# Kernel optimization log

Hardware: AMD Instinct MI355X
Metric: run time of the kernel (lower is better)

## Reference

```python
import jax, jax.numpy as jnp
import numpy as np

B, S, D, H, L, V = 2, 512, 1024, 16, 12, 50257
HD = D // H
DFF = 4 * D


def _ln(x, g, b, eps=1e-5):
    m = jnp.mean(x, axis=-1, keepdims=True)
    v = jnp.var(x, axis=-1, keepdims=True)
    return (x - m) * jax.lax.rsqrt(v + eps) * g + b


def setup_inputs() -> dict:
    key = jax.random.key(0)
    ks = jax.random.split(key, 32)
    sc = 0.02
    n = lambda k, shape: (jax.random.normal(k, shape, dtype=jnp.float32) * sc)
    inp = {
        "input_ids": jax.random.randint(ks[0], (B, S), 0, V, dtype=jnp.int64),
        "attention_mask": jnp.ones((B, S), dtype=jnp.float32),
        "image_hidden_states": jax.random.normal(ks[1], (B, D), dtype=jnp.float32),
        # token embedding table (also used for position embeds and tied lm_head, as in source)
        "wte": n(ks[2], (V, D)),
        # feature_space_transformation_nn: Linear(1024,1024) -> ReLU -> Linear(1024,1024)
        "ft_W1": n(ks[3], (D, D)), "ft_b1": jnp.zeros((D,), jnp.float32),
        "ft_W2": n(ks[4], (D, D)), "ft_b2": jnp.zeros((D,), jnp.float32),
        # per-layer params, stacked on leading L dim
        "ln1_g": jnp.ones((L, D), jnp.float32), "ln1_b": jnp.zeros((L, D), jnp.float32),
        "Wattn": n(ks[5], (L, D, 3 * D)), "battn": jnp.zeros((L, 3 * D), jnp.float32),
        "Wuk": n(ks[6], (L, D, D)), "buk": jnp.zeros((L, D), jnp.float32),
        "Wuv": n(ks[7], (L, D, D)), "buv": jnp.zeros((L, D), jnp.float32),
        "Wproj": n(ks[8], (L, D, D)), "bproj": jnp.zeros((L, D), jnp.float32),
        "ln2_g": jnp.ones((L, D), jnp.float32), "ln2_b": jnp.zeros((L, D), jnp.float32),
        "Wfc": n(ks[9], (L, D, DFF)), "bfc": jnp.zeros((L, DFF), jnp.float32),
        "Wfc2": n(ks[10], (L, DFF, D)), "bfc2": jnp.zeros((L, D), jnp.float32),
        "lnf_g": jnp.ones((D,), jnp.float32), "lnf_b": jnp.zeros((D,), jnp.float32),
    }
    return inp


def _forward(input_ids, attention_mask, image_hidden_states, wte,
             ft_W1, ft_b1, ft_W2, ft_b2,
             ln1_g, ln1_b, Wattn, battn, Wuk, buk, Wuv, buv, Wproj, bproj,
             ln2_g, ln2_b, Wfc, bfc, Wfc2, bfc2, lnf_g, lnf_b):
    # image feature transformation: Linear -> ReLU -> Linear
    img = jax.nn.relu(image_hidden_states @ ft_W1 + ft_b1) @ ft_W2 + ft_b2  # [B,D]

    # NOTE: source uses wte (not wpe) for position embeddings — faithful reproduction
    h = wte[input_ids] + wte[jnp.arange(S)][None]  # [B,S,D]

    # extended attention mask with a prepended zero column for the image token
    mask_ext = (1.0 - attention_mask)[:, None, None, :] * -10000.0  # [B,1,1,S]
    mask_ext = jnp.concatenate([jnp.zeros((B, 1, 1, 1), mask_ext.dtype), mask_ext], axis=-1)  # [B,1,1,S+1]

    # causal mask over kv_len=S+1: query i sees keys j <= i+1 (image token always visible)
    causal = jnp.arange(S + 1)[None, :] <= (jnp.arange(S)[:, None] + 1)  # [S,S+1]

    def block(h, p):
        (l1g, l1b, Wa, ba, Wk, bk, Wv, bv, Wp, bp, l2g, l2b, Wf, bf, Wf2, bf2) = p
        x = _ln(h, l1g, l1b)
        qkv = x @ Wa + ba
        q, k, v = jnp.split(qkv, 3, axis=-1)  # each [B,S,D]
        ki = (img @ Wk + bk)[:, None, :]  # [B,1,D]
        vi = (img @ Wv + bv)[:, None, :]
        k = jnp.concatenate([ki, k], axis=1)  # [B,S+1,D]
        v = jnp.concatenate([vi, v], axis=1)
        sh = lambda t, n: t.reshape(B, n, H, HD).transpose(0, 2, 1, 3)
        qh, kh, vh = sh(q, S), sh(k, S + 1), sh(v, S + 1)
        s = jnp.einsum('bhqd,bhkd->bhqk', qh, kh) / jnp.sqrt(jnp.float32(HD))
        s = jnp.where(causal[None, None], s, jnp.float32(-10000.0))
        s = s + mask_ext
        a = jax.nn.softmax(s, axis=-1)
        o = jnp.einsum('bhqk,bhkd->bhqd', a, vh).transpose(0, 2, 1, 3).reshape(B, S, D)
        h = h + (o @ Wp + bp)
        x = _ln(h, l2g, l2b)
        h = h + (jax.nn.gelu(x @ Wf + bf, approximate=True) @ Wf2 + bf2)
        return h, None

    params = (ln1_g, ln1_b, Wattn, battn, Wuk, buk, Wuv, buv, Wproj, bproj,
              ln2_g, ln2_b, Wfc, bfc, Wfc2, bfc2)
    h, _ = jax.lax.scan(block, h, params)
    h = _ln(h, lnf_g, lnf_b)
    return h @ wte.T  # tied lm head -> [B,S,V]


def reference(input_ids, attention_mask, image_hidden_states, wte,
              ft_W1, ft_b1, ft_W2, ft_b2,
              ln1_g, ln1_b, Wattn, battn, Wuk, buk, Wuv, buv, Wproj, bproj,
              ln2_g, ln2_b, Wfc, bfc, Wfc2, bfc2, lnf_g, lnf_b):
    return _forward(input_ids, attention_mask, image_hidden_states, wte,
                    ft_W1, ft_b1, ft_W2, ft_b2,
                    ln1_g, ln1_b, Wattn, battn, Wuk, buk, Wuv, buv, Wproj, bproj,
                    ln2_g, ln2_b, Wfc, bfc, Wfc2, bfc2, lnf_g, lnf_b)
```

## Files before the change

### kernel.cpp

```cpp
#include <hip/hip_runtime.h>
#include <cstdint>


typedef __bf16 bf16x8 __attribute__((ext_vector_type(8)));
typedef __bf16 bf16x4 __attribute__((ext_vector_type(4)));
typedef float  f32x4  __attribute__((ext_vector_type(4)));

#define GLDS16(g, l) __builtin_amdgcn_global_load_lds( \
    (const __attribute__((address_space(1))) unsigned int*)(g), \
    (__attribute__((address_space(3))) unsigned int*)(l), 16, 0, 0)

#define SCHED_FENCE() __builtin_amdgcn_sched_barrier(0)

__device__ __forceinline__ float gelu_f(float x) {
    float u = 1.5957691216057308f * (x + 0.044715f * x * x * x);
    float e = __expf(u);
    float t = 1.0f - 2.0f / (e + 1.0f);
    return 0.5f * x * (1.0f + t);
}

__device__ __forceinline__ int fragoff(int row, int kh, int hi) {
    return row * 64 + ((kh * 32 + hi * 8) ^ ((row & 7) << 3));
}

__global__ __launch_bounds__(256) void tcvt_layer(
    const float* __restrict__ Wa, const float* __restrict__ Wp,
    const float* __restrict__ Wf, const float* __restrict__ Wf2,
    __bf16* __restrict__ oa, __bf16* __restrict__ op,
    __bf16* __restrict__ of, __bf16* __restrict__ of2)
{
    int id = blockIdx.x;
    const float* src; __bf16* dst; int K, N, kb, nb;
    if (id < 3072)      { src = Wa;  dst = oa;  K = 1024; N = 3072; kb = id & 31;  nb = id >> 5; }
    else if (id < 4096) { id -= 3072; src = Wp;  dst = op;  K = 1024; N = 1024; kb = id & 31;  nb = id >> 5; }
    else if (id < 8192) { id -= 4096; src = Wf;  dst = of;  K = 1024; N = 4096; kb = id & 31;  nb = id >> 5; }
    else                { id -= 8192; src = Wf2; dst = of2; K = 4096; N = 1024; kb = id & 127; nb = id >> 7; }
    const int k0 = kb * 32, n0 = nb * 32;
    __shared__ float tile[32][33];
    const int t = threadIdx.x;
    const int r = t >> 3, c4 = (t & 7) * 4;
    float4 v = *reinterpret_cast<const float4*>(src + (long)(k0 + r) * N + n0 + c4);
    tile[r][c4] = v.x; tile[r][c4 + 1] = v.y; tile[r][c4 + 2] = v.z; tile[r][c4 + 3] = v.w;
    __syncthreads();
    bf16x4 o;
    o[0] = (__bf16)tile[c4][r];
    o[1] = (__bf16)tile[c4 + 1][r];
    o[2] = (__bf16)tile[c4 + 2][r];
    o[3] = (__bf16)tile[c4 + 3][r];
    *reinterpret_cast<bf16x4*>(dst + (long)(n0 + r) * K + k0 + c4) = o;
}

__global__ __launch_bounds__(256) void wcvt(
    const float* __restrict__ wte, __bf16* __restrict__ out, long nvalid)
{
    long e = ((long)blockIdx.x * 256 + threadIdx.x) * 8;
    bf16x8 o;
    if (e < nvalid) {
        float4 a = *reinterpret_cast<const float4*>(wte + e);
        float4 b = *reinterpret_cast<const float4*>(wte + e + 4);
        o[0] = (__bf16)a.x; o[1] = (__bf16)a.y; o[2] = (__bf16)a.z; o[3] = (__bf16)a.w;
        o[4] = (__bf16)b.x; o[5] = (__bf16)b.y; o[6] = (__bf16)b.z; o[7] = (__bf16)b.w;
    } else {
        #pragma unroll
        for (int i = 0; i < 8; i++) o[i] = (__bf16)0.f;
    }
    *reinterpret_cast<bf16x8*>(out + e) = o;
}

__global__ __launch_bounds__(256) void gemv_part(
    const float* __restrict__ x, int xld,
    const float* __restrict__ W, long wzs,
    float* __restrict__ part, int K, int N)
{
    int jb = blockIdx.x, kz = blockIdx.y, z = blockIdx.z;
    int t = threadIdx.x;
    int j = (jb << 6) + (t & 63);
    int g = t >> 6;
    int klen = K / (gridDim.y * 4);
    int kbase = (kz * 4 + g) * klen;
    const float* Wp = W + (long)z * wzs + (long)kbase * N + j;
    const float* x0 = x + kbase;
    const float* x1 = x + xld + kbase;
    float a0 = 0.f, a1 = 0.f;
    for (int k = 0; k < klen; k++) {
        float wv = Wp[(long)k * N];
        a0 += x0[k] * wv;
        a1 += x1[k] * wv;
    }
    __shared__ float r0[4][64], r1[4][64];
    r0[g][t & 63] = a0; r1[g][t & 63] = a1;
    __syncthreads();
    if (t < 64) {
        a0 = r0[0][t] + r0[1][t] + r0[2][t] + r0[3][t];
        a1 = r1[0][t] + r1[1][t] + r1[2][t] + r1[3][t];
        long base = (long)(z * gridDim.y + kz) * 2 * N + (jb << 6) + t;
        part[base]     = a0;
        part[base + N] = a1;
    }
}

__global__ __launch_bounds__(256) void gemv_reduce(
    const float* __restrict__ part, const float* __restrict__ bias, long bzs,
    float* __restrict__ out, int N, int nz, int act)
{
    int idx = blockIdx.x * 256 + threadIdx.x;
    if (idx >= nz * 2 * N) return;
    int j  = idx % N;
    int bz = idx / N;
    int z  = bz >> 1;
    float s = bias[(long)z * bzs + j];
    const float* p = part + ((long)z * 8 * 2 + (bz & 1)) * N + j;
    #pragma unroll
    for (int kz = 0; kz < 8; kz++) s += p[(long)kz * 2 * N];
    if (act) s = fmaxf(s, 0.f);
    out[idx] = s;
}

__global__ __launch_bounds__(256) void gemv_kv_part(
    const float* __restrict__ img,
    const float* __restrict__ Wuk, const float* __restrict__ Wuv,
    float* __restrict__ part)
{
    int jb = blockIdx.x, kz = blockIdx.y, z = blockIdx.z;
    int t = threadIdx.x;
    int j = (jb << 6) + (t & 63);
    int g = t >> 6;
    int kbase = (kz * 4 + g) * 64;
    const float* W = (z < 12) ? (Wuk + (long)z * 1048576) : (Wuv + (long)(z - 12) * 1048576);
    const float* Wp = W + (long)kbase * 1024 + j;
    const float* x0 = img + kbase;
    const float* x1 = img + 1024 + kbase;
    float a0 = 0.f, a1 = 0.f;
    for (int k = 0; k < 64; k++) {
        float wv = Wp[(long)k * 1024];
        a0 += x0[k] * wv;
        a1 += x1[k] * wv;
    }
    __shared__ float r0[4][64], r1[4][64];
    r0[g][t & 63] = a0; r1[g][t & 63] = a1;
    __syncthreads();
    if (t < 64) {
        a0 = r0[0][t] + r0[1][t] + r0[2][t] + r0[3][t];
        a1 = r1[0][t] + r1[1][t] + r1[2][t] + r1[3][t];
        long base = (long)(z * 4 + kz) * 2 * 1024 + (jb << 6) + t;
        part[base]        = a0;
        part[base + 1024] = a1;
    }
}

__global__ __launch_bounds__(256) void gemv_kv_reduce(
    const float* __restrict__ part,
    const float* __restrict__ buk, const float* __restrict__ buv,
    float* __restrict__ imgk, float* __restrict__ imgv)
{
    int idx = blockIdx.x * 256 + threadIdx.x;
    int z = idx >> 11;
    int bsel = (idx >> 10) & 1;
    int j = idx & 1023;
    float s = (z < 12) ? buk[z * 1024 + j] : buv[(z - 12) * 1024 + j];
    const float* p = part + ((long)z * 4 * 2 + bsel) * 1024 + j;
    #pragma unroll
    for (int kz = 0; kz < 4; kz++) s += p[(long)kz * 2 * 1024];
    if (z < 12) imgk[z * 2048 + bsel * 1024 + j] = s;
    else        imgv[(z - 12) * 2048 + bsel * 1024 + j] = s;
}

__global__ __launch_bounds__(256) void embed_ln(
    const int* __restrict__ ids, const float* __restrict__ wte,
    float* __restrict__ h, __bf16* __restrict__ xb,
    const float* __restrict__ g, const float* __restrict__ b)
{
    int row = blockIdx.x;
    int s = row & 511;
    int t = threadIdx.x;
    long id = ids[row];
    float4 v1 = reinterpret_cast<const float4*>(wte + id * 1024)[t];
    float4 v2 = reinterpret_cast<const float4*>(wte + (long)s * 1024)[t];
    float4 v; v.x = v1.x + v2.x; v.y = v1.y + v2.y; v.z = v1.z + v2.z; v.w = v1.w + v2.w;
    reinterpret_cast<float4*>(h + (long)row * 1024)[t] = v;

    float s1 = v.x + v.y + v.z + v.w;
    float s2 = v.x * v.x + v.y * v.y + v.z * v.z + v.w * v.w;
    #pragma unroll
    for (int o = 32; o >= 1; o >>= 1) { s1 += __shfl_xor(s1, o); s2 += __shfl_xor(s2, o); }
    __shared__ float r1[4], r2[4];
    int w = t >> 6;
    if ((t & 63) == 0) { r1[w] = s1; r2[w] = s2; }
    __syncthreads();
    s1 = r1[0] + r1[1] + r1[2] + r1[3];
    s2 = r2[0] + r2[1] + r2[2] + r2[3];
    float mean = s1 * (1.0f / 1024.0f);
    float var  = s2 * (1.0f / 1024.0f) - mean * mean;
    float rstd = rsqrtf(var + 1e-5f);
    float4 gg = reinterpret_cast<const float4*>(g)[t];
    float4 bb = reinterpret_cast<const float4*>(b)[t];
    bf16x4 o;
    o[0] = (__bf16)((v.x - mean) * rstd * gg.x + bb.x);
    o[1] = (__bf16)((v.y - mean) * rstd * gg.y + bb.y);
    o[2] = (__bf16)((v.z - mean) * rstd * gg.z + bb.z);
    o[3] = (__bf16)((v.w - mean) * rstd * gg.w + bb.w);
    *reinterpret_cast<bf16x4*>(xb + (long)row * 1024 + t * 4) = o;
}

__global__ __launch_bounds__(256) void ln_k(
    const float* __restrict__ in, __bf16* __restrict__ out,
    const float* __restrict__ g, const float* __restrict__ b)
{
    int row = blockIdx.x, t = threadIdx.x;
    float4 v = reinterpret_cast<const float4*>(in + (long)row * 1024)[t];
    float s1 = v.x + v.y + v.z + v.w;
    float s2 = v.x * v.x + v.y * v.y + v.z * v.z + v.w * v.w;
    #pragma unroll
    for (int o = 32; o >= 1; o >>= 1) { s1 += __shfl_xor(s1, o); s2 += __shfl_xor(s2, o); }
    __shared__ float r1[4], r2[4];
    int w = t >> 6;
    if ((t & 63) == 0) { r1[w] = s1; r2[w] = s2; }
    __syncthreads();
    s1 = r1[0] + r1[1] + r1[2] + r1[3];
    s2 = r2[0] + r2[1] + r2[2] + r2[3];
    float mean = s1 * (1.0f / 1024.0f);
    float var  = s2 * (1.0f / 1024.0f) - mean * mean;
    float rstd = rsqrtf(var + 1e-5f);
    float4 gg = reinterpret_cast<const float4*>(g)[t];
    float4 bb = reinterpret_cast<const float4*>(b)[t];
    bf16x4 o;
    o[0] = (__bf16)((v.x - mean) * rstd * gg.x + bb.x);
    o[1] = (__bf16)((v.y - mean) * rstd * gg.y + bb.y);
    o[2] = (__bf16)((v.z - mean) * rstd * gg.z + bb.z);
    o[3] = (__bf16)((v.w - mean) * rstd * gg.w + bb.w);
    *reinterpret_cast<bf16x4*>(out + (long)row * 1024 + t * 4) = o;
}

template<int NP>
__global__ __launch_bounds__(256) void lnadd_k(
    float* __restrict__ h, const float* __restrict__ part,
    const float* __restrict__ bias,
    const float* __restrict__ g, const float* __restrict__ b,
    __bf16* __restrict__ out)
{
    int row = blockIdx.x, t = threadIdx.x;
    long off = (long)row * 1024 + t * 4;
    float4 v = *reinterpret_cast<const float4*>(h + off);
    #pragma unroll
    for (int sp = 0; sp < NP; sp++) {
        float4 pv = *reinterpret_cast<const float4*>(part + sp * 1048576L + off);
        v.x += pv.x; v.y += pv.y; v.z += pv.z; v.w += pv.w;
    }
    float4 bi = reinterpret_cast<const float4*>(bias)[t];
    v.x += bi.x; v.y += bi.y; v.z += bi.z; v.w += bi.w;
    *reinterpret_cast<float4*>(h + off) = v;

    float s1 = v.x + v.y + v.z + v.w;
    float s2 = v.x * v.x + v.y * v.y + v.z * v.z + v.w * v.w;
    #pragma unroll
    for (int o = 32; o >= 1; o >>= 1) { s1 += __shfl_xor(s1, o); s2 += __shfl_xor(s2, o); }
    __shared__ float r1[4], r2[4];
    int w = t >> 6;
    if ((t & 63) == 0) { r1[w] = s1; r2[w] = s2; }
    __syncthreads();
    s1 = r1[0] + r1[1] + r1[2] + r1[3];
    s2 = r2[0] + r2[1] + r2[2] + r2[3];
    float mean = s1 * (1.0f / 1024.0f);
    float var  = s2 * (1.0f / 1024.0f) - mean * mean;
    float rstd = rsqrtf(var + 1e-5f);
    float4 gg = reinterpret_cast<const float4*>(g)[t];
    float4 bb = reinterpret_cast<const float4*>(b)[t];
    bf16x4 o;
    o[0] = (__bf16)((v.x - mean) * rstd * gg.x + bb.x);
    o[1] = (__bf16)((v.y - mean) * rstd * gg.y + bb.y);
    o[2] = (__bf16)((v.z - mean) * rstd * gg.z + bb.z);
    o[3] = (__bf16)((v.w - mean) * rstd * gg.w + bb.w);
    *reinterpret_cast<bf16x4*>(out + off) = o;
}

template<int OUTBF16, int ACT, int NBOUND, int PARTIAL>
__global__ __launch_bounds__(256) void gemm128(
    const __bf16* __restrict__ A, const __bf16* __restrict__ Bt,
    const float* __restrict__ bias, void* __restrict__ C,
    int N, int K, int GM, int GN, int NS)
{
    const int total = GM * GN * NS;
    const int q = total >> 3, r = total & 7;
    const int x = blockIdx.x & 7, jj = blockIdx.x >> 3;
    const int w0 = (x < r) ? x * (q + 1) + jj : r * (q + 1) + (x - r) * q + jj;
    const int sp = w0 / (GM * GN);
    const int rem = w0 - sp * (GM * GN);
    const int m0 = (rem % GM) * 128;
    const int n0 = (rem / GM) * 128;

    __shared__ __bf16 As[2][128 * 64];
    __shared__ __bf16 Bs[2][128 * 64];
    const int t = threadIdx.x;
    const int wv = t >> 6, lane = t & 63;
    const int lo = lane & 15, hi = lane >> 4;
    const int wr = wv >> 1, wc = wv & 1;

    f32x4 acc[4][4] = {};

    const int srow = t >> 3;
    const int skx  = (((t & 7) ^ (srow & 7)) << 3);
    const int sldst = t * 8;
    #define ST128(bf, kk) do { \
        _Pragma("unroll") \
        for (int i = 0; i < 4; i++) \
            GLDS16(A + (long)(m0 + i * 32 + srow) * K + (kk) + skx, &As[bf][i * 2048 + sldst]); \
        _Pragma("unroll") \
        for (int i = 0; i < 4; i++) \
            GLDS16(Bt + (long)(n0 + i * 32 + srow) * K + (kk) + skx, &Bs[bf][i * 2048 + sldst]); \
    } while (0)

    const int Ksp = K / NS;
    const int kbeg = sp * Ksp;
    const int T = Ksp >> 6;

    ST128(0, kbeg);
    int cur = 0;
    for (int it = 0; it < T; it++) {
        if (it + 1 < T) {
            ST128(cur ^ 1, kbeg + (it + 1) * 64);
            asm volatile("s_waitcnt vmcnt(8)" ::: "memory");
        } else {
            asm volatile("s_waitcnt vmcnt(0)" ::: "memory");
        }
        SCHED_FENCE();
        __builtin_amdgcn_s_barrier();
        SCHED_FENCE();

        #pragma unroll
        for (int kh = 0; kh < 2; kh++) {
            bf16x8 afr[4], bfr[4];
            #pragma unroll
            for (int mi = 0; mi < 4; mi++)
                afr[mi] = *reinterpret_cast<const bf16x8*>(&As[cur][fragoff(wr * 64 + mi * 16 + lo, kh, hi)]);
            #pragma unroll
            for (int ni = 0; ni < 4; ni++)
                bfr[ni] = *reinterpret_cast<const bf16x8*>(&Bs[cur][fragoff(wc * 64 + ni * 16 + lo, kh, hi)]);
            #pragma unroll
            for (int mi = 0; mi < 4; mi++)
                #pragma unroll
                for (int ni = 0; ni < 4; ni++)
                    acc[mi][ni] = __builtin_amdgcn_mfma_f32_16x16x32_bf16(afr[mi], bfr[ni], acc[mi][ni], 0, 0, 0);
        }

        SCHED_FENCE();
        __builtin_amdgcn_s_barrier();
        SCHED_FENCE();
        cur ^= 1;
    }
    #undef ST128

    const long coff = PARTIAL ? (long)sp * GM * 128 * N : 0;
    #pragma unroll
    for (int mi = 0; mi < 4; mi++)
        #pragma unroll
        for (int ni = 0; ni < 4; ni++) {
            int col = n0 + wc * 64 + ni * 16 + lo;
            if (NBOUND && col >= N) continue;
            float bv = (!PARTIAL && bias) ? bias[col] : 0.f;
            #pragma unroll
            for (int rr = 0; rr < 4; rr++) {
                int row = m0 + wr * 64 + mi * 16 + hi * 4 + rr;
                float v = acc[mi][ni][rr] + bv;
                if (ACT) v = gelu_f(v);
                if (OUTBF16) ((__bf16*)C)[(long)row * N + col] = (__bf16)v;
                else         ((float*)C)[coff + (long)row * N + col] = v;
            }
        }
}

template<int BN, int OUTBF16, int ACT, int PARTIAL>
__global__ __launch_bounds__(256) void gemm64(
    const __bf16* __restrict__ A, const __bf16* __restrict__ Bt,
    const float* __restrict__ bias, void* __restrict__ C,
    int N, int K, int GM, int GN, int NS)
{
    constexpr int NB = BN / 32;
    const int total = GM * GN * NS;
    const int q = total >> 3, r = total & 7;
    const int x = blockIdx.x & 7, jj = blockIdx.x >> 3;
    const int w0 = (x < r) ? x * (q + 1) + jj : r * (q + 1) + (x - r) * q + jj;
    const int sp = w0 / (GM * GN);
    const int rem = w0 - sp * (GM * GN);
    const int m0 = (rem % GM) * 64;
    const int n0 = (rem / GM) * BN;

    __shared__ __bf16 As[2][64 * 64];
    __shared__ __bf16 Bs[2][BN * 64];
    const int t = threadIdx.x;
    const int wv = t >> 6, lane = t & 63;
    const int lo = lane & 15, hi = lane >> 4;
    const int wr = wv >> 1, wc = wv & 1;

    f32x4 acc[2][NB] = {};

    const int srow = t >> 3;
    const int skx  = (((t & 7) ^ (srow & 7)) << 3);
    const int sldst = t * 8;
    #define ST64(bf, kk) do { \
        _Pragma("unroll") \
        for (int i = 0; i < 2; i++) \
            GLDS16(A + (long)(m0 + i * 32 + srow) * K + (kk) + skx, &As[bf][i * 2048 + sldst]); \
        _Pragma("unroll") \
        for (int i = 0; i < NB; i++) \
            GLDS16(Bt + (long)(n0 + i * 32 + srow) * K + (kk) + skx, &Bs[bf][i * 2048 + sldst]); \
    } while (0)

    const int Ksp = K / NS;
    const int kbeg = sp * Ksp;
    const int T = Ksp >> 6;

    ST64(0, kbeg);
    int cur = 0;
    for (int it = 0; it < T; it++) {
        if (it + 1 < T) {
            ST64(cur ^ 1, kbeg + (it + 1) * 64);
            if constexpr (NB == 4) asm volatile("s_waitcnt vmcnt(6)" ::: "memory");
            else                   asm volatile("s_waitcnt vmcnt(4)" ::: "memory");
        } else {
            asm volatile("s_waitcnt vmcnt(0)" ::: "memory");
        }
        SCHED_FENCE();
        __builtin_amdgcn_s_barrier();
        SCHED_FENCE();

        #pragma unroll
        for (int kh = 0; kh < 2; kh++) {
            bf16x8 afr[2], bfr[NB];
            #pragma unroll
            for (int mi = 0; mi < 2; mi++)
                afr[mi] = *reinterpret_cast<const bf16x8*>(&As[cur][fragoff(wr * 32 + mi * 16 + lo, kh, hi)]);
            #pragma unroll
            for (int ni = 0; ni < NB; ni++)
                bfr[ni] = *reinterpret_cast<const bf16x8*>(&Bs[cur][fragoff(wc * (BN / 2) + ni * 16 + lo, kh, hi)]);
            #pragma unroll
            for (int mi = 0; mi < 2; mi++)
                #pragma unroll
                for (int ni = 0; ni < NB; ni++)
                    acc[mi][ni] = __builtin_amdgcn_mfma_f32_16x16x32_bf16(afr[mi], bfr[ni], acc[mi][ni], 0, 0, 0);
        }

        SCHED_FENCE();
        __builtin_amdgcn_s_barrier();
        SCHED_FENCE();
        cur ^= 1;
    }
    #undef ST64

    const long coff = PARTIAL ? (long)sp * GM * 64 * N : 0;
    #pragma unroll
    for (int mi = 0; mi < 2; mi++)
        #pragma unroll
        for (int ni = 0; ni < NB; ni++) {
            int col = n0 + wc * (BN / 2) + ni * 16 + lo;
            float bv = (!PARTIAL && bias) ? bias[col] : 0.f;
            #pragma unroll
            for (int rr = 0; rr < 4; rr++) {
                int row = m0 + wr * 32 + mi * 16 + hi * 4 + rr;
                float v = acc[mi][ni][rr] + bv;
                if (ACT) v = gelu_f(v);
                if (OUTBF16) ((__bf16*)C)[(long)row * N + col] = (__bf16)v;
                else         ((float*)C)[coff + (long)row * N + col] = v;
            }
        }
}

template<int OUTBF16, int ACT, int RES>
__global__ __launch_bounds__(256) void gemm_bb(
    const __bf16* __restrict__ A, const __bf16* __restrict__ Bt,
    const float* __restrict__ bias, const float* __restrict__ res,
    void* __restrict__ C, int N, int K)
{
    __shared__ __bf16 As[64 * 32];
    __shared__ __bf16 Bs[64 * 32];
    const int t = threadIdx.x;
    const int m0 = blockIdx.x * 64;
    const int n0 = blockIdx.y * 64;
    const int w = t >> 6, lane = t & 63;
    const int lo = lane & 15, hi = lane >> 4;
    const int wr = w >> 1, wc = w & 1;

    f32x4 acc[2][2] = {};

    for (int k0 = 0; k0 < K; k0 += 32) {
        __syncthreads();
        GLDS16(A  + (long)(m0 + (t >> 2)) * K + k0 + ((t & 3) << 3), &As[t * 8]);
        GLDS16(Bt + (long)(n0 + (t >> 2)) * K + k0 + ((t & 3) << 3), &Bs[t * 8]);
        __syncthreads();
        bf16x8 afr[2], bfr[2];
        #pragma unroll
        for (int mi = 0; mi < 2; mi++)
            afr[mi] = *reinterpret_cast<const bf16x8*>(&As[(wr * 32 + mi * 16 + lo) * 32 + hi * 8]);
        #pragma unroll
        for (int ni = 0; ni < 2; ni++)
            bfr[ni] = *reinterpret_cast<const bf16x8*>(&Bs[(wc * 32 + ni * 16 + lo) * 32 + hi * 8]);
        #pragma unroll
        for (int mi = 0; mi < 2; mi++)
            #pragma unroll
            for (int ni = 0; ni < 2; ni++)
                acc[mi][ni] = __builtin_amdgcn_mfma_f32_16x16x32_bf16(afr[mi], bfr[ni], acc[mi][ni], 0, 0, 0);
    }

    #pragma unroll
    for (int mi = 0; mi < 2; mi++)
        #pragma unroll
        for (int ni = 0; ni < 2; ni++) {
            int col = n0 + wc * 32 + ni * 16 + lo;
            float bv = bias ? bias[col] : 0.f;
            #pragma unroll
            for (int rr = 0; rr < 4; rr++) {
                int row = m0 + wr * 32 + mi * 16 + hi * 4 + rr;
                float v = acc[mi][ni][rr] + bv;
                if (ACT) v = gelu_f(v);
                if (RES) v += res[(long)row * N + col];
                if (OUTBF16) ((__bf16*)C)[(long)row * N + col] = (__bf16)v;
                else         ((float*)C)[(long)row * N + col] = v;
            }
        }
}

__global__ __launch_bounds__(256) void gemm_lm(
    const __bf16* __restrict__ A, const float* __restrict__ Wt,
    float* __restrict__ C, int N, int K)
{
    __shared__ __bf16 As[128 * 32];
    __shared__ __bf16 Bs[128 * 32];
    const int t = threadIdx.x;
    const int m0 = blockIdx.x * 128;
    const int n0 = blockIdx.y * 128;
    const int w = t >> 6, lane = t & 63;
    const int lo = lane & 15, hi = lane >> 4;
    const int wr = w >> 1, wc = w & 1;

    f32x4 acc[4][4] = {};

    for (int k0 = 0; k0 < K; k0 += 32) {
        __syncthreads();
        #pragma unroll
        for (int i = 0; i < 2; i++) {
            int c = i * 256 + t;
            GLDS16(A + (long)(m0 + (c >> 2)) * K + k0 + ((c & 3) << 3), &As[c * 8]);
        }
        #pragma unroll
        for (int i = 0; i < 2; i++) {
            int c = i * 256 + t;
            int nr = n0 + (c >> 2);
            bf16x8 bv;
            if (nr < N) {
                const float* wp = Wt + (long)nr * K + k0 + ((c & 3) << 3);
                float4 b0 = *reinterpret_cast<const float4*>(wp);
                float4 b1 = *reinterpret_cast<const float4*>(wp + 4);
                bv[0] = (__bf16)b0.x; bv[1] = (__bf16)b0.y; bv[2] = (__bf16)b0.z; bv[3] = (__bf16)b0.w;
                bv[4] = (__bf16)b1.x; bv[5] = (__bf16)b1.y; bv[6] = (__bf16)b1.z; bv[7] = (__bf16)b1.w;
            } else {
                #pragma unroll
                for (int qq = 0; qq < 8; qq++) bv[qq] = (__bf16)0.f;
            }
            *reinterpret_cast<bf16x8*>(&Bs[c * 8]) = bv;
        }
        __syncthreads();
        bf16x8 afr[4], bfr[4];
        #pragma unroll
        for (int mi = 0; mi < 4; mi++)
            afr[mi] = *reinterpret_cast<const bf16x8*>(&As[(wr * 64 + mi * 16 + lo) * 32 + hi * 8]);
        #pragma unroll
        for (int ni = 0; ni < 4; ni++)
            bfr[ni] = *reinterpret_cast<const bf16x8*>(&Bs[(wc * 64 + ni * 16 + lo) * 32 + hi * 8]);
        #pragma unroll
        for (int mi = 0; mi < 4; mi++)
            #pragma unroll
            for (int ni = 0; ni < 4; ni++)
                acc[mi][ni] = __builtin_amdgcn_mfma_f32_16x16x32_bf16(afr[mi], bfr[ni], acc[mi][ni], 0, 0, 0);
    }

    #pragma unroll
    for (int mi = 0; mi < 4; mi++)
        #pragma unroll
        for (int ni = 0; ni < 4; ni++) {
            int col = n0 + wc * 64 + ni * 16 + lo;
            if (col < N) {
                #pragma unroll
                for (int rr = 0; rr < 4; rr++) {
                    int row = m0 + wr * 64 + mi * 16 + hi * 4 + rr;
                    C[(long)row * N + col] = acc[mi][ni][rr];
                }
            }
        }
}

__global__ __launch_bounds__(256) void attn_mfma(
    const __bf16* __restrict__ qkv,
    const float* __restrict__ imgk, const float* __restrict__ imgv,
    const float* __restrict__ amask, __bf16* __restrict__ out)
{
    const int qb = blockIdx.x;
    const int h  = blockIdx.y;
    const int b  = blockIdx.z;
    const int t = threadIdx.x, w = t >> 6, lane = t & 63;
    const int lo = lane & 15, hi = lane >> 4;

    __shared__ __bf16 Ks[64][72];
    __shared__ __bf16 Vt[64][72];
    __shared__ __bf16 Ps[4][16][72];
    __shared__ float kimg_s[64];
    __shared__ float amv_s[64];

    const int kr8 = t >> 2, kd8 = (t & 3) * 16;
    const int vr8 = t & 63, vd8 = (t >> 6) * 16;

    const __bf16* qrow = qkv + (long)(b * 512 + qb * 64 + w * 16 + lo) * 3072 + h * 64;
    bf16x8 qf0 = *reinterpret_cast<const bf16x8*>(qrow + hi * 8);
    bf16x8 qf1 = *reinterpret_cast<const bf16x8*>(qrow + 32 + hi * 8);

    if (t < 64) kimg_s[t] = imgk[b * 1024 + h * 64 + t];
    __syncthreads();

    float simg = 0.f;
    #pragma unroll
    for (int i = 0; i < 8; i++)
        simg += (float)qf0[i] * kimg_s[hi * 8 + i] + (float)qf1[i] * kimg_s[32 + hi * 8 + i];
    simg += __shfl_xor(simg, 16);
    simg += __shfl_xor(simg, 32);
    simg *= 0.125f;

    float pimg[4], l_part[4];
    f32x4 o_acc[4];
    #pragma unroll
    for (int rr = 0; rr < 4; rr++) {
        pimg[rr] = __expf(__shfl(simg, hi * 4 + rr));
        l_part[rr] = 0.f;
    }
    #pragma unroll
    for (int df = 0; df < 4; df++) {
        float vi = imgv[b * 1024 + h * 64 + df * 16 + lo];
        #pragma unroll
        for (int rr = 0; rr < 4; rr++) o_acc[df][rr] = pimg[rr] * vi;
    }

    bf16x8 ck0, ck1, cv0, cv1;
    {
        const __bf16* ks = qkv + (long)(b * 512 + kr8) * 3072 + 1024 + h * 64 + kd8;
        ck0 = *reinterpret_cast<const bf16x8*>(ks);
        ck1 = *reinterpret_cast<const bf16x8*>(ks + 8);
        const __bf16* vs = qkv + (long)(b * 512 + vr8) * 3072 + 2048 + h * 64 + vd8;
        cv0 = *reinterpret_cast<const bf16x8*>(vs);
        cv1 = *reinterpret_cast<const bf16x8*>(vs + 8);
    }

    for (int kb = 0; kb <= qb; kb++) {
        bf16x8 nk0, nk1, nv0, nv1;
        const bool more = (kb < qb);
        if (more) {
            const __bf16* ks = qkv + (long)(b * 512 + (kb + 1) * 64 + kr8) * 3072 + 1024 + h * 64 + kd8;
            nk0 = *reinterpret_cast<const bf16x8*>(ks);
            nk1 = *reinterpret_cast<const bf16x8*>(ks + 8);
            const __bf16* vs = qkv + (long)(b * 512 + (kb + 1) * 64 + vr8) * 3072 + 2048 + h * 64 + vd8;
            nv0 = *reinterpret_cast<const bf16x8*>(vs);
            nv1 = *reinterpret_cast<const bf16x8*>(vs + 8);
        }
        __syncthreads();
        *reinterpret_cast<bf16x8*>(&Ks[kr8][kd8])     = ck0;
        *reinterpret_cast<bf16x8*>(&Ks[kr8][kd8 + 8]) = ck1;
        #pragma unroll
        for (int i = 0; i < 8; i++) { Vt[vd8 + i][vr8] = cv0[i]; Vt[vd8 + 8 + i][vr8] = cv1[i]; }
        if (t < 64) amv_s[t] = (1.0f - amask[b * 512 + kb * 64 + t]) * -10000.0f;
        __syncthreads();

        f32x4 sf[4];
        #pragma unroll
        for (int js = 0; js < 4; js++) {
            bf16x8 kf0 = *reinterpret_cast<const bf16x8*>(&Ks[js * 16 + lo][hi * 8]);
            bf16x8 kf1 = *reinterpret_cast<const bf16x8*>(&Ks[js * 16 + lo][32 + hi * 8]);
            f32x4 a = {};
            a = __builtin_amdgcn_mfma_f32_16x16x32_bf16(qf0, kf0, a, 0, 0, 0);
            a = __builtin_amdgcn_mfma_f32_16x16x32_bf16(qf1, kf1, a, 0, 0, 0);
            sf[js] = a;
        }
        #pragma unroll
        for (int js = 0; js < 4; js++) {
            float amv = amv_s[js * 16 + lo];
            #pragma unroll
            for (int rr = 0; rr < 4; rr++) {
                float sv = sf[js][rr] * 0.125f + amv;
                if (kb == qb) {
                    int qrw = w * 16 + hi * 4 + rr;
                    if (js * 16 + lo > qrw) sv = -10000.0f + amv;
                }
                float p = __expf(sv);
                l_part[rr] += p;
                Ps[w][hi * 4 + rr][js * 16 + lo] = (__bf16)p;
            }
        }
        #pragma unroll
        for (int jb = 0; jb < 2; jb++) {
            bf16x8 pf = *reinterpret_cast<const bf16x8*>(&Ps[w][lo][jb * 32 + hi * 8]);
            #pragma unroll
            for (int df = 0; df < 4; df++) {
                bf16x8 vf = *reinterpret_cast<const bf16x8*>(&Vt[df * 16 + lo][jb * 32 + hi * 8]);
                o_acc[df] = __builtin_amdgcn_mfma_f32_16x16x32_bf16(pf, vf, o_acc[df], 0, 0, 0);
            }
        }
        if (more) { ck0 = nk0; ck1 = nk1; cv0 = nv0; cv1 = nv1; }
    }

    float linv[4];
    #pragma unroll
    for (int rr = 0; rr < 4; rr++) {
        float ls = l_part[rr];
        #pragma unroll
        for (int off = 1; off < 16; off <<= 1) ls += __shfl_xor(ls, off);
        linv[rr] = 1.0f / (pimg[rr] + ls);
    }
    #pragma unroll
    for (int df = 0; df < 4; df++)
        #pragma unroll
        for (int rr = 0; rr < 4; rr++) {
            long row = b * 512 + qb * 64 + w * 16 + hi * 4 + rr;
            out[row * 1024 + h * 64 + df * 16 + lo] = (__bf16)(o_acc[df][rr] * linv[rr]);
        }
}

extern "C" void kernel_launch(void* const* d_in, const int* in_sizes, int n_in,
                              void* d_out, int out_size, void* d_ws, size_t ws_size,
                              hipStream_t stream) {
    (void)in_sizes; (void)n_in; (void)out_size;
    const int*   ids   = (const int*)d_in[0];
    const float* amask = (const float*)d_in[1];
    const float* ihs   = (const float*)d_in[2];
    const float* wte   = (const float*)d_in[3];
    const float* ftW1  = (const float*)d_in[4];
    const float* ftb1  = (const float*)d_in[5];
    const float* ftW2  = (const float*)d_in[6];
    const float* ftb2  = (const float*)d_in[7];
    const float* ln1g  = (const float*)d_in[8];
    const float* ln1b  = (const float*)d_in[9];
    const float* Wattn = (const float*)d_in[10];
    const float* battn = (const float*)d_in[11];
    const float* Wuk   = (const float*)d_in[12];
    const float* buk   = (const float*)d_in[13];
    const float* Wuv   = (const float*)d_in[14];
    const float* buv   = (const float*)d_in[15];
    const float* Wproj = (const float*)d_in[16];
    const float* bproj = (const float*)d_in[17];
    const float* ln2g  = (const float*)d_in[18];
    const float* ln2b  = (const float*)d_in[19];
    const float* Wfc   = (const float*)d_in[20];
    const float* bfc   = (const float*)d_in[21];
    const float* Wfc2  = (const float*)d_in[22];
    const float* bfc2  = (const float*)d_in[23];
    const float* lnfg  = (const float*)d_in[24];
    const float* lnfb  = (const float*)d_in[25];
    float* out = (float*)d_out;

    const long VP = 50304;
    char* base = (char*)d_ws;
    float* ftmp  = (float*)(base);
    float* img   = (float*)(base + (1 << 13));
    float* imgk  = (float*)(base + (1 << 14));
    float* imgv  = (float*)(base + 114688);
    float* part  = (float*)(base + 212992);
    float* h     = (float*)(base + 1048576);
    char* p = base + 5 * 1048576;
    __bf16* xb    = (__bf16*)p; p += 2 * 1048576;
    __bf16* qkvb  = (__bf16*)p; p += 6 * 1048576;
    __bf16* attob = (__bf16*)p; p += 2 * 1048576;
    __bf16* ffb   = (__bf16*)p; p += 8 * 1048576;
    __bf16* wtA   = (__bf16*)p; p += 6 * 1048576;
    __bf16* wtP   = (__bf16*)p; p += 2 * 1048576;
    __bf16* wtF   = (__bf16*)p; p += 8 * 1048576;
    __bf16* wtF2  = (__bf16*)p; p += 8 * 1048576;
    __bf16* wteb  = (__bf16*)p;
    size_t need1 = (size_t)(p - base) + (size_t)VP * 1024 * 2;
    float* part_g = (float*)(base + need1);
    size_t need2 = need1 + 4 * 1048576 * sizeof(float);
    const bool big_ws  = (ws_size >= need1);
    const bool big_ws2 = (ws_size >= need2);

    dim3 b256(256);

    gemv_part<<<dim3(16, 8, 1), b256, 0, stream>>>(ihs, 1024, ftW1, 0, part, 1024, 1024);
    gemv_reduce<<<dim3(8), b256, 0, stream>>>(part, ftb1, 0, ftmp, 1024, 1, 1);
    gemv_part<<<dim3(16, 8, 1), b256, 0, stream>>>(ftmp, 1024, ftW2, 0, part, 1024, 1024);
    gemv_reduce<<<dim3(8), b256, 0, stream>>>(part, ftb2, 0, img, 1024, 1, 0);
    gemv_kv_part<<<dim3(16, 4, 24), b256, 0, stream>>>(img, Wuk, Wuv, part);
    gemv_kv_reduce<<<dim3(192), b256, 0, stream>>>(part, buk, buv, imgk, imgv);

    embed_ln<<<dim3(1024), b256, 0, stream>>>(ids, wte, h, xb, ln1g, ln1b);

    for (int l = 0; l < 12; l++) {
        tcvt_layer<<<dim3(12288), b256, 0, stream>>>(
            Wattn + (long)l * 1024 * 3072, Wproj + (long)l * 1024 * 1024,
            Wfc + (long)l * 1024 * 4096, Wfc2 + (long)l * 4096 * 1024,
            wtA, wtP, wtF, wtF2);

        gemm64<128, 1, 0, 0><<<dim3(384), b256, 0, stream>>>(
            xb, wtA, battn + l * 3072, qkvb, 3072, 1024, 16, 24, 1);
        attn_mfma<<<dim3(8, 16, 2), b256, 0, stream>>>(
            qkvb, imgk + l * 2048, imgv + l * 2048, amask, attob);

        const float* ng = (l < 11) ? (ln1g + (l + 1) * 1024) : lnfg;
        const float* nb = (l < 11) ? (ln1b + (l + 1) * 1024) : lnfb;
        if (big_ws2) {
            gemm64<64, 0, 0, 1><<<dim3(512), b256, 0, stream>>>(
                attob, wtP, nullptr, part_g, 1024, 1024, 16, 16, 2);
            lnadd_k<2><<<dim3(1024), b256, 0, stream>>>(
                h, part_g, bproj + l * 1024, ln2g + l * 1024, ln2b + l * 1024, xb);
            gemm64<128, 1, 1, 0><<<dim3(512), b256, 0, stream>>>(
                xb, wtF, bfc + l * 4096, ffb, 4096, 1024, 16, 32, 1);
            gemm64<128, 0, 0, 1><<<dim3(512), b256, 0, stream>>>(
                ffb, wtF2, nullptr, part_g, 1024, 4096, 16, 8, 4);
            lnadd_k<4><<<dim3(1024), b256, 0, stream>>>(
                h, part_g, bfc2 + l * 1024, ng, nb, xb);
        } else {
            gemm_bb<0, 0, 1><<<dim3(16, 16), b256, 0, stream>>>(
                attob, wtP, bproj + l * 1024, h, h, 1024, 1024);
            ln_k<<<dim3(1024), b256, 0, stream>>>(h, xb, ln2g + l * 1024, ln2b + l * 1024);
            gemm64<128, 1, 1, 0><<<dim3(512), b256, 0, stream>>>(
                xb, wtF, bfc + l * 4096, ffb, 4096, 1024, 16, 32, 1);
            gemm_bb<0, 0, 1><<<dim3(16, 16), b256, 0, stream>>>(
                ffb, wtF2, bfc2 + l * 1024, h, h, 1024, 4096);
            ln_k<<<dim3(1024), b256, 0, stream>>>(h, xb, ng, nb);
        }
    }

    if (big_ws) {
        wcvt<<<dim3((unsigned)(VP * 1024 / 2048)), b256, 0, stream>>>(wte, wteb, 50257L * 1024);
        gemm128<0, 0, 1, 0><<<dim3(3144), b256, 0, stream>>>(
            xb, wteb, nullptr, out, 50257, 1024, 8, 393, 1);
    } else {
        gemm_lm<<<dim3(8, 393), b256, 0, stream>>>(xb, wte, out, 50257, 1024);
    }
}
```

Before: 1.593 ms.

## Overlap weight conversion with attention and enlarge LM-head GEMM tiles

Next-layer weight transpose/convert (and the vocab embedding conversion on the final layer) are folded into the attention launch as extra blocks. This lets the conversion run alongside the small 256-block attention grid, using double-buffered converted-weight workspaces. The transpose kernel now works on 64x64 tiles, and the LM head uses a new 256x256-tile, 512-thread GEMM with padded vocab. The cost is more workspace, a larger shared-memory footprint for attention, and possible register pressure in the bigger GEMM.

```diff
diff --git a/kernel.cpp b/kernel.cpp
--- a/kernel.cpp
+++ b/kernel.cpp
@@ -23,48 +23,73 @@
     return row * 64 + ((kh * 32 + hi * 8) ^ ((row & 7) << 3));
 }
 
-__global__ __launch_bounds__(256) void tcvt_layer(
+__device__ __forceinline__ void tcvt_body(
+    int id, const float* __restrict__ Wa, const float* __restrict__ Wp,
+    const float* __restrict__ Wf, const float* __restrict__ Wf2,
+    __bf16* __restrict__ oa, __bf16* __restrict__ op,
+    __bf16* __restrict__ of, __bf16* __restrict__ of2, float* tile)
+{
+    const float* src; __bf16* dst; int K, N, kb, nb;
+    if (id < 768)       { src = Wa;  dst = oa;  K = 1024; N = 3072; kb = id & 15; nb = id >> 4; }
+    else if (id < 1024) { id -= 768;  src = Wp;  dst = op;  K = 1024; N = 1024; kb = id & 15; nb = id >> 4; }
+    else if (id < 2048) { id -= 1024; src = Wf;  dst = of;  K = 1024; N = 4096; kb = id & 15; nb = id >> 4; }
+    else                { id -= 2048; src = Wf2; dst = of2; K = 4096; N = 1024; kb = id & 63; nb = id >> 6; }
+    const int k0 = kb * 64, n0 = nb * 64;
+    const int t = threadIdx.x;
+    #pragma unroll
+    for (int i = 0; i < 4; i++) {
+        int r = i * 16 + (t >> 4), c = (t & 15) * 4;
+        float4 v = *reinterpret_cast<const float4*>(src + (long)(k0 + r) * N + n0 + c);
+        tile[r * 65 + c] = v.x; tile[r * 65 + c + 1] = v.y;
+        tile[r * 65 + c + 2] = v.z; tile[r * 65 + c + 3] = v.w;
+    }
+    __syncthreads();
+    const int nrow = t >> 2, kc = (t & 3) * 16;
+    bf16x8 o0, o1;
+    #pragma unroll
+    for (int i = 0; i < 8; i++) {
+        o0[i] = (__bf16)tile[(kc + i) * 65 + nrow];
+        o1[i] = (__bf16)tile[(kc + 8 + i) * 65 + nrow];
+    }
+    *reinterpret_cast<bf16x8*>(dst + (long)(n0 + nrow) * K + k0 + kc)     = o0;
+    *reinterpret_cast<bf16x8*>(dst + (long)(n0 + nrow) * K + k0 + kc + 8) = o1;
+}
+
+__device__ __forceinline__ void wcvt_body(
+    int id, const float* __restrict__ wte, __bf16* __restrict__ out, long nvalid)
+{
+    long base = (long)id * 8192 + threadIdx.x * 8;
+    #pragma unroll
+    for (int i = 0; i < 4; i++) {
+        long e = base + (long)i * 2048;
+        bf16x8 o;
+        if (e < nvalid) {
+            float4 a = *reinterpret_cast<const float4*>(wte + e);
+            float4 b = *reinterpret_cast<const float4*>(wte + e + 4);
+            o[0] = (__bf16)a.x; o[1] = (__bf16)a.y; o[2] = (__bf16)a.z; o[3] = (__bf16)a.w;
+            o[4] = (__bf16)b.x; o[5] = (__bf16)b.y; o[6] = (__bf16)b.z; o[7] = (__bf16)b.w;
+        } else {
+            #pragma unroll
+            for (int q = 0; q < 8; q++) o[q] = (__bf16)0.f;
+        }
+        *reinterpret_cast<bf16x8*>(out + e) = o;
+    }
+}
+
+__global__ __launch_bounds__(256) void tcvt_std(
     const float* __restrict__ Wa, const float* __restrict__ Wp,
     const float* __restrict__ Wf, const float* __restrict__ Wf2,
     __bf16* __restrict__ oa, __bf16* __restrict__ op,
     __bf16* __restrict__ of, __bf16* __restrict__ of2)
 {
-    int id = blockIdx.x;
-    const float* src; __bf16* dst; int K, N, kb, nb;
-    if (id < 3072)      { src = Wa;  dst = oa;  K = 1024; N = 3072; kb = id & 31;  nb = id >> 5; }
-    else if (id < 4096) { id -= 3072; src = Wp;  dst = op;  K = 1024; N = 1024; kb = id & 31;  nb = id >> 5; }
-    else if (id < 8192) { id -= 4096; src = Wf;  dst = of;  K = 1024; N = 4096; kb = id & 31;  nb = id >> 5; }
-    else                { id -= 8192; src = Wf2; dst = of2; K = 4096; N = 1024; kb = id & 127; nb = id >> 7; }
-    const int k0 = kb * 32, n0 = nb * 32;
-    __shared__ float tile[32][33];
-    const int t = threadIdx.x;
-    const int r = t >> 3, c4 = (t & 7) * 4;
-    float4 v = *reinterpret_cast<const float4*>(src + (long)(k0 + r) * N + n0 + c4);
-    tile[r][c4] = v.x; tile[r][c4 + 1] = v.y; tile[r][c4 + 2] = v.z; tile[r][c4 + 3] = v.w;
-    __syncthreads();
-    bf16x4 o;
-    o[0] = (__bf16)tile[c4][r];
-    o[1] = (__bf16)tile[c4 + 1][r];
-    o[2] = (__bf16)tile[c4 + 2][r];
-    o[3] = (__bf16)tile[c4 + 3][r];
-    *reinterpret_cast<bf16x4*>(dst + (long)(n0 + r) * K + k0 + c4) = o;
-}
-
-__global__ __launch_bounds__(256) void wcvt(
+    __shared__ float tile[64 * 65];
+    tcvt_body(blockIdx.x, Wa, Wp, Wf, Wf2, oa, op, of, of2, tile);
+}
+
+__global__ __launch_bounds__(256) void wcvt_std(
     const float* __restrict__ wte, __bf16* __restrict__ out, long nvalid)
 {
-    long e = ((long)blockIdx.x * 256 + threadIdx.x) * 8;
-    bf16x8 o;
-    if (e < nvalid) {
-        float4 a = *reinterpret_cast<const float4*>(wte + e);
-        float4 b = *reinterpret_cast<const float4*>(wte + e + 4);
-        o[0] = (__bf16)a.x; o[1] = (__bf16)a.y; o[2] = (__bf16)a.z; o[3] = (__bf16)a.w;
-        o[4] = (__bf16)b.x; o[5] = (__bf16)b.y; o[6] = (__bf16)b.z; o[7] = (__bf16)b.w;
-    } else {
-        #pragma unroll
-        for (int i = 0; i < 8; i++) o[i] = (__bf16)0.f;
-    }
-    *reinterpret_cast<bf16x8*>(out + e) = o;
+    wcvt_body(blockIdx.x, wte, out, nvalid);
 }
 
 __global__ __launch_bounds__(256) void gemv_part(
@@ -273,51 +298,44 @@
     *reinterpret_cast<bf16x4*>(out + off) = o;
 }
 
-template<int OUTBF16, int ACT, int NBOUND, int PARTIAL>
-__global__ __launch_bounds__(256) void gemm128(
+__global__ __launch_bounds__(512) void gemm256(
     const __bf16* __restrict__ A, const __bf16* __restrict__ Bt,
-    const float* __restrict__ bias, void* __restrict__ C,
-    int N, int K, int GM, int GN, int NS)
-{
-    const int total = GM * GN * NS;
+    float* __restrict__ C, int N, int K, int GM, int GN)
+{
+    const int total = GM * GN;
     const int q = total >> 3, r = total & 7;
     const int x = blockIdx.x & 7, jj = blockIdx.x >> 3;
     const int w0 = (x < r) ? x * (q + 1) + jj : r * (q + 1) + (x - r) * q + jj;
-    const int sp = w0 / (GM * GN);
-    const int rem = w0 - sp * (GM * GN);
-    const int m0 = (rem % GM) * 128;
-    const int n0 = (rem / GM) * 128;
-
-    __shared__ __bf16 As[2][128 * 64];
-    __shared__ __bf16 Bs[2][128 * 64];
+    const int m0 = (w0 % GM) * 256;
+    const int n0 = (w0 / GM) * 256;
+
+    __shared__ __bf16 As[2][256 * 64];
+    __shared__ __bf16 Bs[2][256 * 64];
     const int t = threadIdx.x;
-    const int wv = t >> 6, lane = t & 63;
+    const int wid = t >> 6, lane = t & 63;
     const int lo = lane & 15, hi = lane >> 4;
-    const int wr = wv >> 1, wc = wv & 1;
-
-    f32x4 acc[4][4] = {};
+    const int wr = wid >> 2, wc = wid & 3;
+
+    f32x4 acc[8][4] = {};
 
     const int srow = t >> 3;
     const int skx  = (((t & 7) ^ (srow & 7)) << 3);
     const int sldst = t * 8;
-    #define ST128(bf, kk) do { \
+    #define ST256(bf, kk) do { \
         _Pragma("unroll") \
         for (int i = 0; i < 4; i++) \
-            GLDS16(A + (long)(m0 + i * 32 + srow) * K + (kk) + skx, &As[bf][i * 2048 + sldst]); \
+            GLDS16(A + (long)(m0 + i * 64 + srow) * K + (kk) + skx, &As[bf][i * 4096 + sldst]); \
         _Pragma("unroll") \
         for (int i = 0; i < 4; i++) \
-            GLDS16(Bt + (long)(n0 + i * 32 + srow) * K + (kk) + skx, &Bs[bf][i * 2048 + sldst]); \
+            GLDS16(Bt + (long)(n0 + i * 64 + srow) * K + (kk) + skx, &Bs[bf][i * 4096 + sldst]); \
     } while (0)
 
-    const int Ksp = K / NS;
-    const int kbeg = sp * Ksp;
-    const int T = Ksp >> 6;
-
-    ST128(0, kbeg);
+    const int T = K >> 6;
+    ST256(0, 0);
     int cur = 0;
     for (int it = 0; it < T; it++) {
         if (it + 1 < T) {
-            ST128(cur ^ 1, kbeg + (it + 1) * 64);
+            ST256(cur ^ 1, (it + 1) * 64);
             asm volatile("s_waitcnt vmcnt(8)" ::: "memory");
         } else {
             asm volatile("s_waitcnt vmcnt(0)" ::: "memory");
@@ -328,15 +346,15 @@
 
         #pragma unroll
         for (int kh = 0; kh < 2; kh++) {
-            bf16x8 afr[4], bfr[4];
-            #pragma unroll
-            for (int mi = 0; mi < 4; mi++)
-                afr[mi] = *reinterpret_cast<const bf16x8*>(&As[cur][fragoff(wr * 64 + mi * 16 + lo, kh, hi)]);
+            bf16x8 afr[8], bfr[4];
+            #pragma unroll
+            for (int mi = 0; mi < 8; mi++)
+                afr[mi] = *reinterpret_cast<const bf16x8*>(&As[cur][fragoff(wr * 128 + mi * 16 + lo, kh, hi)]);
             #pragma unroll
             for (int ni = 0; ni < 4; ni++)
                 bfr[ni] = *reinterpret_cast<const bf16x8*>(&Bs[cur][fragoff(wc * 64 + ni * 16 + lo, kh, hi)]);
             #pragma unroll
-            for (int mi = 0; mi < 4; mi++)
+            for (int mi = 0; mi < 8; mi++)
                 #pragma unroll
                 for (int ni = 0; ni < 4; ni++)
                     acc[mi][ni] = __builtin_amdgcn_mfma_f32_16x16x32_bf16(afr[mi], bfr[ni], acc[mi][ni], 0, 0, 0);
@@ -347,23 +365,18 @@
         SCHED_FENCE();
         cur ^= 1;
     }
-    #undef ST128
-
-    const long coff = PARTIAL ? (long)sp * GM * 128 * N : 0;
-    #pragma unroll
-    for (int mi = 0; mi < 4; mi++)
+    #undef ST256
+
+    #pragma unroll
+    for (int mi = 0; mi < 8; mi++)
         #pragma unroll
         for (int ni = 0; ni < 4; ni++) {
             int col = n0 + wc * 64 + ni * 16 + lo;
-            if (NBOUND && col >= N) continue;
-            float bv = (!PARTIAL && bias) ? bias[col] : 0.f;
+            if (col >= N) continue;
             #pragma unroll
             for (int rr = 0; rr < 4; rr++) {
-                int row = m0 + wr * 64 + mi * 16 + hi * 4 + rr;
-                float v = acc[mi][ni][rr] + bv;
-                if (ACT) v = gelu_f(v);
-                if (OUTBF16) ((__bf16*)C)[(long)row * N + col] = (__bf16)v;
-                else         ((float*)C)[coff + (long)row * N + col] = v;
+                int row = m0 + wr * 128 + mi * 16 + hi * 4 + rr;
+                C[(long)row * N + col] = acc[mi][ni][rr];
             }
         }
 }
@@ -587,22 +600,38 @@
         }
 }
 
-__global__ __launch_bounds__(256) void attn_mfma(
+__global__ __launch_bounds__(256) void attn_aux(
     const __bf16* __restrict__ qkv,
     const float* __restrict__ imgk, const float* __restrict__ imgv,
-    const float* __restrict__ amask, __bf16* __restrict__ out)
-{
-    const int qb = blockIdx.x;
-    const int h  = blockIdx.y;
-    const int b  = blockIdx.z;
+    const float* __restrict__ amask, __bf16* __restrict__ out,
+    int aux_mode,
+    const float* __restrict__ Wa, const float* __restrict__ Wp,
+    const float* __restrict__ Wf, const float* __restrict__ Wf2,
+    __bf16* __restrict__ oa, __bf16* __restrict__ op,
+    __bf16* __restrict__ of, __bf16* __restrict__ of2,
+    const float* __restrict__ wte, __bf16* __restrict__ wteb, long nvalid)
+{
+    __shared__ __align__(16) char smem[28416];
+    const int bid = blockIdx.x;
+    if (bid >= 256) {
+        if (aux_mode == 1)
+            tcvt_body(bid - 256, Wa, Wp, Wf, Wf2, oa, op, of, of2, (float*)smem);
+        else
+            wcvt_body(bid - 256, wte, wteb, nvalid);
+        return;
+    }
+
+    __bf16 (*Ks)[72] = (__bf16(*)[72])(smem);
+    __bf16 (*Vt)[72] = (__bf16(*)[72])(smem + 9216);
+    __bf16 (*Ps)[16][72] = (__bf16(*)[16][72])(smem + 18432);
+    float* kimg_s = (float*)(smem + 27648);
+    float* amv_s  = (float*)(smem + 27904);
+
+    const int qb = bid & 7;
+    const int h  = (bid >> 3) & 15;
+    const int b  = bid >> 7;
     const int t = threadIdx.x, w = t >> 6, lane = t & 63;
     const int lo = lane & 15, hi = lane >> 4;
-
-    __shared__ __bf16 Ks[64][72];
-    __shared__ __bf16 Vt[64][72];
-    __shared__ __bf16 Ps[4][16][72];
-    __shared__ float kimg_s[64];
-    __shared__ float amv_s[64];
 
     const int kr8 = t >> 2, kd8 = (t & 3) * 16;
     const int vr8 = t & 63, vd8 = (t >> 6) * 16;
@@ -751,7 +780,8 @@
     const float* lnfb  = (const float*)d_in[25];
     float* out = (float*)d_out;
 
-    const long VP = 50304;
+    const long VP2 = 50432;
+    const long NVALID = 50257L * 1024;
     char* base = (char*)d_ws;
     float* ftmp  = (float*)(base);
     float* img   = (float*)(base + (1 << 13));
@@ -764,16 +794,28 @@
     __bf16* qkvb  = (__bf16*)p; p += 6 * 1048576;
     __bf16* attob = (__bf16*)p; p += 2 * 1048576;
     __bf16* ffb   = (__bf16*)p; p += 8 * 1048576;
-    __bf16* wtA   = (__bf16*)p; p += 6 * 1048576;
-    __bf16* wtP   = (__bf16*)p; p += 2 * 1048576;
-    __bf16* wtF   = (__bf16*)p; p += 8 * 1048576;
-    __bf16* wtF2  = (__bf16*)p; p += 8 * 1048576;
-    __bf16* wteb  = (__bf16*)p;
-    size_t need1 = (size_t)(p - base) + (size_t)VP * 1024 * 2;
+    __bf16* wtA0  = (__bf16*)p; p += 6 * 1048576;
+    __bf16* wtP0  = (__bf16*)p; p += 2 * 1048576;
+    __bf16* wtF0  = (__bf16*)p; p += 8 * 1048576;
+    __bf16* wtF20 = (__bf16*)p; p += 8 * 1048576;
+    __bf16* wteb  = (__bf16*)p; p += VP2 * 1024 * 2;
+    size_t need1 = (size_t)(p - base);
     float* part_g = (float*)(base + need1);
     size_t need2 = need1 + 4 * 1048576 * sizeof(float);
-    const bool big_ws  = (ws_size >= need1);
-    const bool big_ws2 = (ws_size >= need2);
+    char* p2 = base + need2;
+    __bf16* wtA1  = (__bf16*)p2; p2 += 6 * 1048576;
+    __bf16* wtP1  = (__bf16*)p2; p2 += 2 * 1048576;
+    __bf16* wtF1  = (__bf16*)p2; p2 += 8 * 1048576;
+    __bf16* wtF21 = (__bf16*)p2; p2 += 8 * 1048576;
+    size_t need3 = (size_t)(p2 - base);
+    const bool big1 = (ws_size >= need1);
+    const bool big2 = (ws_size >= need2);
+    const bool big3 = (ws_size >= need3);
+
+    __bf16* wtA_s[2]  = {wtA0, wtA1};
+    __bf16* wtP_s[2]  = {wtP0, wtP1};
+    __bf16* wtF_s[2]  = {wtF0, wtF1};
+    __bf16* wtF2_s[2] = {wtF20, wtF21};
 
     dim3 b256(256);
 
@@ -785,47 +827,78 @@
     gemv_kv_reduce<<<dim3(192), b256, 0, stream>>>(part, buk, buv, imgk, imgv);
 
     embed_ln<<<dim3(1024), b256, 0, stream>>>(ids, wte, h, xb, ln1g, ln1b);
+    tcvt_std<<<dim3(3072), b256, 0, stream>>>(
+        Wattn, Wproj, Wfc, Wfc2, wtA0, wtP0, wtF0, wtF20);
 
     for (int l = 0; l < 12; l++) {
-        tcvt_layer<<<dim3(12288), b256, 0, stream>>>(
-            Wattn + (long)l * 1024 * 3072, Wproj + (long)l * 1024 * 1024,
-            Wfc + (long)l * 1024 * 4096, Wfc2 + (long)l * 4096 * 1024,
-            wtA, wtP, wtF, wtF2);
+        const int cs = big3 ? (l & 1) : 0;
+        __bf16* cA  = wtA_s[cs];
+        __bf16* cP  = wtP_s[cs];
+        __bf16* cF  = wtF_s[cs];
+        __bf16* cF2 = wtF2_s[cs];
+
+        if (!big3 && l > 0) {
+            tcvt_std<<<dim3(3072), b256, 0, stream>>>(
+                Wattn + (long)l * 1024 * 3072, Wproj + (long)l * 1024 * 1024,
+                Wfc + (long)l * 1024 * 4096, Wfc2 + (long)l * 4096 * 1024,
+                wtA0, wtP0, wtF0, wtF20);
+        }
 
         gemm64<128, 1, 0, 0><<<dim3(384), b256, 0, stream>>>(
-            xb, wtA, battn + l * 3072, qkvb, 3072, 1024, 16, 24, 1);
-        attn_mfma<<<dim3(8, 16, 2), b256, 0, stream>>>(
-            qkvb, imgk + l * 2048, imgv + l * 2048, amask, attob);
+            xb, cA, battn + l * 3072, qkvb, 3072, 1024, 16, 24, 1);
+
+        if (big3 && l < 11) {
+            const int ns = (l + 1) & 1;
+            attn_aux<<<dim3(256 + 3072), b256, 0, stream>>>(
+                qkvb, imgk + l * 2048, imgv + l * 2048, amask, attob, 1,
+                Wattn + (long)(l + 1) * 1024 * 3072, Wproj + (long)(l + 1) * 1024 * 1024,
+                Wfc + (long)(l + 1) * 1024 * 4096, Wfc2 + (long)(l + 1) * 4096 * 1024,
+                wtA_s[ns], wtP_s[ns], wtF_s[ns], wtF2_s[ns],
+                nullptr, nullptr, 0);
+        } else if (big3 && l == 11) {
+            attn_aux<<<dim3(256 + 6304), b256, 0, stream>>>(
+                qkvb, imgk + l * 2048, imgv + l * 2048, amask, attob, 2,
+                nullptr, nullptr, nullptr, nullptr,
+                nullptr, nullptr, nullptr, nullptr,
+                wte, wteb, NVALID);
+        } else {
+            attn_aux<<<dim3(256), b256, 0, stream>>>(
+                qkvb, imgk + l * 2048, imgv + l * 2048, amask, attob, 0,
+                nullptr, nullptr, nullptr, nullptr,
+                nullptr, nullptr, nullptr, nullptr,
+                nullptr, nullptr, 0);
+        }
 
         const float* ng = (l < 11) ? (ln1g + (l + 1) * 1024) : lnfg;
         const float* nb = (l < 11) ? (ln1b + (l + 1) * 1024) : lnfb;
-        if (big_ws2) {
+        if (big2) {
             gemm64<64, 0, 0, 1><<<dim3(512), b256, 0, stream>>>(
-                attob, wtP, nullptr, part_g, 1024, 1024, 16, 16, 2);
+                attob, cP, nullptr, part_g, 1024, 1024, 16, 16, 2);
             lnadd_k<2><<<dim3(1024), b256, 0, stream>>>(
                 h, part_g, bproj + l * 1024, ln2g + l * 1024, ln2b + l * 1024, xb);
             gemm64<128, 1, 1, 0><<<dim3(512), b256, 0, stream>>>(
-                xb, wtF, bfc + l * 4096, ffb, 4096, 1024, 16, 32, 1);
+                xb, cF, bfc + l * 4096, ffb, 4096, 1024, 16, 32, 1);
             gemm64<128, 0, 0, 1><<<dim3(512), b256, 0, stream>>>(
-                ffb, wtF2, nullptr, part_g, 1024, 4096, 16, 8, 4);
+                ffb, cF2, nullptr, part_g, 1024, 4096, 16, 8, 4);
             lnadd_k<4><<<dim3(1024), b256, 0, stream>>>(
                 h, part_g, bfc2 + l * 1024, ng, nb, xb);
         } else {
             gemm_bb<0, 0, 1><<<dim3(16, 16), b256, 0, stream>>>(
-                attob, wtP, bproj + l * 1024, h, h, 1024, 1024);
+                attob, cP, bproj + l * 1024, h, h, 1024, 1024);
             ln_k<<<dim3(1024), b256, 0, stream>>>(h, xb, ln2g + l * 1024, ln2b + l * 1024);
             gemm64<128, 1, 1, 0><<<dim3(512), b256, 0, stream>>>(
-                xb, wtF, bfc + l * 4096, ffb, 4096, 1024, 16, 32, 1);
+                xb, cF, bfc + l * 4096, ffb, 4096, 1024, 16, 32, 1);
             gemm_bb<0, 0, 1><<<dim3(16, 16), b256, 0, stream>>>(
-                ffb, wtF2, bfc2 + l * 1024, h, h, 1024, 4096);
+                ffb, cF2, bfc2 + l * 1024, h, h, 1024, 4096);
             ln_k<<<dim3(1024), b256, 0, stream>>>(h, xb, ng, nb);
         }
     }
 
-    if (big_ws) {
-        wcvt<<<dim3((unsigned)(VP * 1024 / 2048)), b256, 0, stream>>>(wte, wteb, 50257L * 1024);
-        gemm128<0, 0, 1, 0><<<dim3(3144), b256, 0, stream>>>(
-            xb, wteb, nullptr, out, 50257, 1024, 8, 393, 1);
+    if (big1) {
+        if (!big3)
+            wcvt_std<<<dim3((unsigned)(VP2 * 1024 / 8192)), b256, 0, stream>>>(wte, wteb, NVALID);
+        gemm256<<<dim3(788), dim3(512), 0, stream>>>(
+            xb, wteb, out, 50257, 1024, 4, (int)(VP2 / 256));
     } else {
         gemm_lm<<<dim3(8, 393), b256, 0, stream>>>(xb, wte, out, 50257, 1024);
     }
```

After: 1.474 ms. 1.08x faster.
